# Kernel optimization log

Measured on AMD Instinct MI355X. Metric: run time of the kernel, lower is better.

Reference implementation:

```python
import jax, jax.numpy as jnp
import numpy as np

L = (7, 5, 5, 5, 5)            # num_quantized_values (all odd -> exact product codebook)
LATENT_DIM = len(L)
MAX_SEQ_LEN = 2048
LATENT_SEQ_LEN = 1024
CODEBOOK_SIZE = int(np.prod(L))  # 4375


def build_codebook():
    # Matches build_codebook_recursive: dim 0 varies slowest ('ij' meshgrid + ravel).
    ranges = [jnp.arange(-(l // 2), l // 2 + 1, dtype=jnp.int32) for l in L]
    grids = jnp.meshgrid(*ranges, indexing='ij')
    return jnp.stack([g.ravel() for g in grids], axis=-1)  # [K, D] int32


def setup_inputs() -> dict:
    key = jax.random.key(0)
    k1, k2, k3 = jax.random.split(key, 3)
    B, S, D = 16, MAX_SEQ_LEN, 1024
    x = jax.random.normal(k1, (B, S, D), dtype=jnp.float32)
    W_enc = jax.random.normal(k2, (D, LATENT_DIM), dtype=jnp.float32) / np.sqrt(D)
    W_dec = jax.random.normal(k3, (LATENT_DIM, D), dtype=jnp.float32) / np.sqrt(LATENT_DIM)
    return {"x": x, "W_enc": W_enc, "W_dec": W_dec}


def reference(x, W_enc, W_dec):
    B, S, _ = x.shape
    codebook = build_codebook()                                   # [K, D_lat]
    half = jnp.array([l // 2 for l in L], dtype=jnp.float32)      # (L/2).int()

    # encode: stand-in linear encoder, then zero tokens past latent_seq_len
    h = jnp.einsum('bsd,de->bse', x, W_enc)                        # [B,S,D_lat]
    mask = (jnp.arange(S) < LATENT_SEQ_LEN)[None, :, None]
    h = h * mask
    z_e = h.reshape(-1, LATENT_DIM)                                # [N, D_lat]

    # quantize: FSQ tanh squash + round with straight-through estimator
    z_e_sq = half * jnp.tanh(z_e)
    z_q = jnp.round(z_e_sq)
    z = jax.lax.stop_gradient(z_q - z_e_sq) + z_e_sq

    # brute-force codebook index lookup: [N,1,D] == [K,D] -> all -> argmax
    matches = jnp.all(z.astype(jnp.int32)[:, None, :] == codebook[None], axis=-1)  # [N,K]
    idx = jnp.argmax(matches, axis=1)                              # [N]

    # codebook usage (fresh zero-initialized usage buffer)
    used = jnp.zeros((CODEBOOK_SIZE,), dtype=jnp.float32).at[idx].set(1.0)
    unique = jnp.sum(used)
    usage = (unique + (CODEBOOK_SIZE - unique) * jnp.exp(jnp.float32(-1.0))) / CODEBOOK_SIZE

    # decode: stand-in linear decoder
    z3 = z.reshape(-1, MAX_SEQ_LEN, LATENT_DIM)                    # [B, num_latents, D_lat]
    x_out = jnp.einsum('bse,ed->bsd', z3, W_dec)                   # [B,S,D]
    percent_masked = jnp.float32(0.0)

    return x_out, z_e, z_q, usage, unique.astype(jnp.int32), percent_masked
```

## Files before the change

kernel.cpp:

```cpp
#include <hip/hip_runtime.h>

#define MAX_SEQ   2048
#define LAT_SEQ   1024
#define DIM       1024
#define DLAT      5
#define K_CB      4375
#define ZERO_IDX  2187


__global__ void prep(const float* __restrict__ Wenc,
                     float* __restrict__ WencT,
                     int* __restrict__ used) {
    int i = blockIdx.x * blockDim.x + threadIdx.x;
    if (i < 5120) {
        int e = i >> 10, d = i & 1023;
        WencT[i] = Wenc[d * DLAT + e];
    }
    if (i < K_CB) used[i] = (i == ZERO_IDX) ? 1 : 0;
}

__global__ __launch_bounds__(256) void fsq_main(
    const float* __restrict__ x,
    const float* __restrict__ WencT,
    const float* __restrict__ Wdec,
    float* __restrict__ xout,
    float* __restrict__ ze,
    float* __restrict__ zq,
    int*   __restrict__ used)
{
    const int wave = threadIdx.x >> 6;
    const int lane = threadIdx.x & 63;
    const int u    = blockIdx.x * 4 + wave;
    const int b    = u >> 10;
    const int s    = u & 1023;
    const int t    = b * MAX_SEQ + s;
    const int tm   = t + LAT_SEQ;
    const long long row  = (long long)t  * DIM;
    const long long rowm = (long long)tm * DIM;

    float4 v[4];
    #pragma unroll
    for (int q = 0; q < 4; ++q)
        v[q] = *(const float4*)(x + row + q * 256 + lane * 4);

    {
        const float4 z4 = make_float4(0.f, 0.f, 0.f, 0.f);
        #pragma unroll
        for (int q = 0; q < 4; ++q)
            *(float4*)(xout + rowm + q * 256 + lane * 4) = z4;
        if (lane < DLAT) {
            ze[tm * DLAT + lane] = 0.f;
            zq[tm * DLAT + lane] = 0.f;
        }
    }

    float acc[DLAT] = {0.f, 0.f, 0.f, 0.f, 0.f};
    #pragma unroll
    for (int q = 0; q < 4; ++q) {
        const int c0 = q * 256 + lane * 4;
        #pragma unroll
        for (int e = 0; e < DLAT; ++e) {
            const float4 w = *(const float4*)(WencT + e * DIM + c0);
            acc[e] += v[q].x * w.x + v[q].y * w.y + v[q].z * w.z + v[q].w * w.w;
        }
    }
    #pragma unroll
    for (int e = 0; e < DLAT; ++e) {
        float a = acc[e];
        #pragma unroll
        for (int o = 32; o > 0; o >>= 1) a += __shfl_xor(a, o, 64);
        acc[e] = a;
    }

    const float halfv[DLAT] = {3.f, 2.f, 2.f, 2.f, 2.f};
    float zqv[DLAT];
    int   ci[DLAT];
    #pragma unroll
    for (int e = 0; e < DLAT; ++e) {
        const float zsq = halfv[e] * tanhf(acc[e]);
        zqv[e] = rintf(zsq);
        ci[e]  = (int)zqv[e];
    }

    if (lane < DLAT) {
        ze[t * DLAT + lane] = acc[lane];
        zq[t * DLAT + lane] = zqv[lane];
    }
    if (lane == 0) {
        const int idx = ((((ci[0] + 3) * 5 + (ci[1] + 2)) * 5 + (ci[2] + 2)) * 5
                          + (ci[3] + 2)) * 5 + (ci[4] + 2);
        used[idx] = 1;
    }

    #pragma unroll
    for (int q = 0; q < 4; ++q) {
        const int c0 = q * 256 + lane * 4;
        float4 o = make_float4(0.f, 0.f, 0.f, 0.f);
        #pragma unroll
        for (int e = 0; e < DLAT; ++e) {
            const float4 w = *(const float4*)(Wdec + e * DIM + c0);
            o.x += zqv[e] * w.x; o.y += zqv[e] * w.y;
            o.z += zqv[e] * w.z; o.w += zqv[e] * w.w;
        }
        *(float4*)(xout + row + c0) = o;
    }
}

__global__ void finalize(const int* __restrict__ used, float* __restrict__ scal) {
    __shared__ int sh[256];
    const int t = threadIdx.x;
    int sum = 0;
    for (int i = t; i < K_CB; i += 256) sum += used[i];
    sh[t] = sum;
    __syncthreads();
    for (int o = 128; o > 0; o >>= 1) {
        if (t < o) sh[t] += sh[t + o];
        __syncthreads();
    }
    if (t == 0) {
        const float uniq  = (float)sh[0];
        const float usage = (uniq + ((float)K_CB - uniq) * expf(-1.0f)) / (float)K_CB;
        scal[0] = usage;
        scal[1] = uniq;
        scal[2] = 0.0f;
    }
}

extern "C" void kernel_launch(void* const* d_in, const int* in_sizes, int n_in,
                              void* d_out, int out_size, void* d_ws, size_t ws_size,
                              hipStream_t stream) {
    const float* x    = (const float*)d_in[0];
    const float* Wenc = (const float*)d_in[1];
    const float* Wdec = (const float*)d_in[2];

    float* out  = (float*)d_out;
    float* xout = out;
    float* ze   = out + 33554432;
    float* zq   = ze + 163840;
    float* scal = zq + 163840;

    int*   used  = (int*)d_ws;
    float* WencT = (float*)d_ws + 8192;

    prep<<<20, 256, 0, stream>>>(Wenc, WencT, used);
    fsq_main<<<4096, 256, 0, stream>>>(x, WencT, Wdec, xout, ze, zq, used);
    finalize<<<1, 256, 0, stream>>>(used, scal);
}
```

Measured before the change: 46.95 us.

## Process two tokens per wave, stage weights in LDS, drop prep kernel

Each wave now handles two token rows, so weight loads are amortized over twice the work and the grid is halved. Encoder (transposed) and decoder weights are staged in shared memory per block instead of read from global/workspace. The separate prep kernel is replaced by a memset, and the zero-code usage entry is patched in finalize. This trades per-block weight staging (40KB LDS, strided Wenc gather) and lower occupancy for fewer launches and more reuse.

```diff
diff --git a/kernel.cpp b/kernel.cpp
--- a/kernel.cpp
+++ b/kernel.cpp
@@ -7,102 +7,129 @@
 #define K_CB      4375
 #define ZERO_IDX  2187
 
-
-__global__ void prep(const float* __restrict__ Wenc,
-                     float* __restrict__ WencT,
-                     int* __restrict__ used) {
-    int i = blockIdx.x * blockDim.x + threadIdx.x;
-    if (i < 5120) {
-        int e = i >> 10, d = i & 1023;
-        WencT[i] = Wenc[d * DLAT + e];
-    }
-    if (i < K_CB) used[i] = (i == ZERO_IDX) ? 1 : 0;
-}
-
 __global__ __launch_bounds__(256) void fsq_main(
     const float* __restrict__ x,
-    const float* __restrict__ WencT,
+    const float* __restrict__ Wenc,
     const float* __restrict__ Wdec,
     float* __restrict__ xout,
     float* __restrict__ ze,
     float* __restrict__ zq,
     int*   __restrict__ used)
 {
-    const int wave = threadIdx.x >> 6;
-    const int lane = threadIdx.x & 63;
-    const int u    = blockIdx.x * 4 + wave;
-    const int b    = u >> 10;
-    const int s    = u & 1023;
-    const int t    = b * MAX_SEQ + s;
-    const int tm   = t + LAT_SEQ;
-    const long long row  = (long long)t  * DIM;
-    const long long rowm = (long long)tm * DIM;
+    __shared__ float wencT[DLAT * DIM];
+    __shared__ float wdecS[DLAT * DIM];
 
-    float4 v[4];
+    const int tid  = threadIdx.x;
+    const int wave = tid >> 6;
+    const int lane = tid & 63;
+    const int u0   = (blockIdx.x * 4 + wave) * 2;
+
+    int t[2];  long long row[2], rowm[2];
     #pragma unroll
-    for (int q = 0; q < 4; ++q)
-        v[q] = *(const float4*)(x + row + q * 256 + lane * 4);
+    for (int p = 0; p < 2; ++p) {
+        const int u = u0 + p;
+        const int b = u >> 10, s = u & 1023;
+        t[p]    = b * MAX_SEQ + s;
+        row[p]  = (long long)t[p] * DIM;
+        rowm[p] = row[p] + (long long)LAT_SEQ * DIM;
+    }
 
-    {
-        const float4 z4 = make_float4(0.f, 0.f, 0.f, 0.f);
+    float4 v[2][4];
+    #pragma unroll
+    for (int p = 0; p < 2; ++p)
         #pragma unroll
         for (int q = 0; q < 4; ++q)
-            *(float4*)(xout + rowm + q * 256 + lane * 4) = z4;
+            v[p][q] = *(const float4*)(x + row[p] + q * 256 + lane * 4);
+
+    const float4 z4 = make_float4(0.f, 0.f, 0.f, 0.f);
+    #pragma unroll
+    for (int p = 0; p < 2; ++p) {
+        #pragma unroll
+        for (int q = 0; q < 4; ++q)
+            *(float4*)(xout + rowm[p] + q * 256 + lane * 4) = z4;
         if (lane < DLAT) {
+            const int tm = t[p] + LAT_SEQ;
             ze[tm * DLAT + lane] = 0.f;
             zq[tm * DLAT + lane] = 0.f;
         }
     }
 
-    float acc[DLAT] = {0.f, 0.f, 0.f, 0.f, 0.f};
+    {
+        const float4* src = (const float4*)Wdec;
+        float4*       dst = (float4*)wdecS;
+        #pragma unroll
+        for (int m = 0; m < 5; ++m)
+            dst[tid + 256 * m] = src[tid + 256 * m];
+        #pragma unroll
+        for (int m = 0; m < 20; ++m) {
+            const int k = tid + 256 * m;
+            const int e = k >> 10, d = k & 1023;
+            wencT[k] = Wenc[d * DLAT + e];
+        }
+    }
+    __syncthreads();
+
+    float acc[2][DLAT] = {};
     #pragma unroll
     for (int q = 0; q < 4; ++q) {
         const int c0 = q * 256 + lane * 4;
         #pragma unroll
         for (int e = 0; e < DLAT; ++e) {
-            const float4 w = *(const float4*)(WencT + e * DIM + c0);
-            acc[e] += v[q].x * w.x + v[q].y * w.y + v[q].z * w.z + v[q].w * w.w;
+            const float4 w = *(const float4*)(wencT + e * DIM + c0);
+            #pragma unroll
+            for (int p = 0; p < 2; ++p)
+                acc[p][e] += v[p][q].x * w.x + v[p][q].y * w.y
+                           + v[p][q].z * w.z + v[p][q].w * w.w;
         }
     }
     #pragma unroll
-    for (int e = 0; e < DLAT; ++e) {
-        float a = acc[e];
+    for (int p = 0; p < 2; ++p)
         #pragma unroll
-        for (int o = 32; o > 0; o >>= 1) a += __shfl_xor(a, o, 64);
-        acc[e] = a;
-    }
+        for (int e = 0; e < DLAT; ++e) {
+            float a = acc[p][e];
+            #pragma unroll
+            for (int o = 32; o > 0; o >>= 1) a += __shfl_xor(a, o, 64);
+            acc[p][e] = a;
+        }
 
     const float halfv[DLAT] = {3.f, 2.f, 2.f, 2.f, 2.f};
-    float zqv[DLAT];
-    int   ci[DLAT];
+    float zqv[2][DLAT];
     #pragma unroll
-    for (int e = 0; e < DLAT; ++e) {
-        const float zsq = halfv[e] * tanhf(acc[e]);
-        zqv[e] = rintf(zsq);
-        ci[e]  = (int)zqv[e];
-    }
-
-    if (lane < DLAT) {
-        ze[t * DLAT + lane] = acc[lane];
-        zq[t * DLAT + lane] = zqv[lane];
-    }
-    if (lane == 0) {
-        const int idx = ((((ci[0] + 3) * 5 + (ci[1] + 2)) * 5 + (ci[2] + 2)) * 5
-                          + (ci[3] + 2)) * 5 + (ci[4] + 2);
-        used[idx] = 1;
+    for (int p = 0; p < 2; ++p) {
+        int ci[DLAT];
+        #pragma unroll
+        for (int e = 0; e < DLAT; ++e) {
+            const float zsq = halfv[e] * tanhf(acc[p][e]);
+            zqv[p][e] = rintf(zsq);
+            ci[e]     = (int)zqv[p][e];
+        }
+        if (lane < DLAT) {
+            ze[t[p] * DLAT + lane] = acc[p][lane];
+            zq[t[p] * DLAT + lane] = zqv[p][lane];
+        }
+        if (lane == 0) {
+            const int idx = ((((ci[0] + 3) * 5 + (ci[1] + 2)) * 5 + (ci[2] + 2)) * 5
+                              + (ci[3] + 2)) * 5 + (ci[4] + 2);
+            used[idx] = 1;
+        }
     }
 
     #pragma unroll
     for (int q = 0; q < 4; ++q) {
         const int c0 = q * 256 + lane * 4;
-        float4 o = make_float4(0.f, 0.f, 0.f, 0.f);
+        float4 o[2] = {make_float4(0.f,0.f,0.f,0.f), make_float4(0.f,0.f,0.f,0.f)};
         #pragma unroll
         for (int e = 0; e < DLAT; ++e) {
-            const float4 w = *(const float4*)(Wdec + e * DIM + c0);
-            o.x += zqv[e] * w.x; o.y += zqv[e] * w.y;
-            o.z += zqv[e] * w.z; o.w += zqv[e] * w.w;
+            const float4 w = *(const float4*)(wdecS + e * DIM + c0);
+            #pragma unroll
+            for (int p = 0; p < 2; ++p) {
+                o[p].x += zqv[p][e] * w.x; o[p].y += zqv[p][e] * w.y;
+                o[p].z += zqv[p][e] * w.z; o[p].w += zqv[p][e] * w.w;
+            }
         }
-        *(float4*)(xout + row + c0) = o;
+        #pragma unroll
+        for (int p = 0; p < 2; ++p)
+            *(float4*)(xout + row[p] + c0) = o[p];
     }
 }
 
@@ -118,7 +145,7 @@
         __syncthreads();
     }
     if (t == 0) {
-        const float uniq  = (float)sh[0];
+        const float uniq  = (float)sh[0] + (used[ZERO_IDX] ? 0.f : 1.f);
         const float usage = (uniq + ((float)K_CB - uniq) * expf(-1.0f)) / (float)K_CB;
         scal[0] = usage;
         scal[1] = uniq;
@@ -139,10 +166,9 @@
     float* zq   = ze + 163840;
     float* scal = zq + 163840;
 
-    int*   used  = (int*)d_ws;
-    float* WencT = (float*)d_ws + 8192;
+    int* used = (int*)d_ws;
 
-    prep<<<20, 256, 0, stream>>>(Wenc, WencT, used);
-    fsq_main<<<4096, 256, 0, stream>>>(x, WencT, Wdec, xout, ze, zq, used);
+    hipMemsetAsync(used, 0, K_CB * sizeof(int), stream);
+    fsq_main<<<2048, 256, 0, stream>>>(x, Wenc, Wdec, xout, ze, zq, used);
     finalize<<<1, 256, 0, stream>>>(used, scal);
 }
```

Measured after the change: 44.90 us. 1.05x faster.
